# Performance work log

Hardware: AMD Instinct MI355X
Metric: run time of the kernel (lower is better)

The kernel has to match this reference:

```python
import jax, jax.numpy as jnp
import numpy as np

THETA = 0.02


def _low_texture_mask(tgt_img):
    # grad magnitudes averaged over channels
    gx = jnp.mean(jnp.abs(tgt_img[:, :, :, :-1] - tgt_img[:, :, :, 1:]), axis=1, keepdims=True)
    gy = jnp.mean(jnp.abs(tgt_img[:, :, :-1, :] - tgt_img[:, :, 1:, :]), axis=1, keepdims=True)
    tw = jnp.zeros_like(tgt_img[:, :1, :, :])
    tw = tw.at[:, :, :, :-1].add(gx)
    tw = tw.at[:, :, :-1, :].add(gy)
    tw = tw / 2.0
    return tw < jnp.mean(tw)  # [B,1,H,W] bool: low-texture == invalid


def _forward(pred_depth, gt_depth, tgt_img, u_rand):
    B, C, H, W = gt_depth.shape
    N = H * W
    invalid = _low_texture_mask(tgt_img).reshape(B, N)          # bool [B,N]
    valid = ~invalid
    gt = gt_depth.reshape(B, N)
    pred = pred_depth.reshape(B, N)

    # Uniform sampling among valid pixels per batch (inverse-CDF on cumsum).
    vcum = jnp.cumsum(valid.astype(jnp.int32), axis=1)          # [B,N]
    nval = vcum[:, -1:]                                         # [B,1]
    u = jnp.minimum((u_rand * nval.astype(u_rand.dtype)).astype(jnp.int32), nval - 1)
    idx = jax.vmap(lambda c, uu: jnp.searchsorted(c, uu, side='right'))(vcum, u)  # [B,N]

    gt_val = jnp.take_along_axis(gt, idx, axis=1)               # z_B ground truth
    pred_val = jnp.take_along_axis(pred, idx, axis=1)           # z_B prediction

    # Relative-depth target for (invalid pixel, sampled valid pixel) pairs
    r1 = gt / gt_val
    r2 = gt_val / gt
    target = jnp.where(r1 >= 1.0 + THETA, 1.0,
                       jnp.where(r2 > 1.0 + THETA, -1.0, 0.0))

    d = pred - pred_val                                         # z_A - z_B
    nz = invalid & (target != 0.0)
    zz = invalid & (target == 0.0)

    arg = jnp.where(nz, -target * d, 0.0)
    log_loss = jnp.sum(jnp.where(nz, jnp.log1p(jnp.exp(arg)), 0.0)) / jnp.sum(nz).astype(d.dtype)
    sq_loss = jnp.sum(jnp.where(zz, d * d, 0.0)) / jnp.sum(zz).astype(d.dtype)
    return log_loss + sq_loss


def setup_inputs() -> dict:
    key = jax.random.key(0)
    k1, k2, k3, k4 = jax.random.split(key, 4)
    B, H, W = 16, 512, 1024
    pred_depth = jax.random.normal(k1, (B, 1, H, W), dtype=jnp.float32)
    gt_depth = jax.random.uniform(k2, (B, 1, H, W), dtype=jnp.float32, minval=0.01, maxval=1.0)
    tgt_img = jax.random.uniform(k3, (B, 3, H, W), dtype=jnp.float32)
    u_rand = jax.random.uniform(k4, (B, H * W), dtype=jnp.float32)
    return {"pred_depth": pred_depth, "gt_depth": gt_depth, "tgt_img": tgt_img, "u_rand": u_rand}


def reference(pred_depth, gt_depth, tgt_img, u_rand):
    return _forward(pred_depth, gt_depth, tgt_img, u_rand)
```

## Files before the change

kernel.cpp:

```cpp
#include <hip/hip_runtime.h>
#include <hip/hip_bf16.h>
#include <math.h>

#define BB 16
#define CC 3
#define HH 512
#define WW 1024
#define NN (HH * WW)
#define BN ((size_t)BB * NN)

typedef __attribute__((ext_vector_type(4))) _Float16 half4;
typedef __attribute__((ext_vector_type(2))) _Float16 h2;
typedef __attribute__((ext_vector_type(4))) float f4;


__device__ __forceinline__ void tw4(const float* __restrict__ img, size_t g0, float out[4]) {
    int w0 = (int)(g0 & (WW - 1));
    int h  = (int)((g0 >> 10) & (HH - 1));
    int b  = (int)(g0 >> 19);
    const float* p = img + (size_t)b * CC * NN + (size_t)h * WW + w0;
    float c0[5], c1[5], c2[5], d0[4], d1[4], d2[4];
    f4 v;
    v = *(const f4*)p;            c0[0]=v.x; c0[1]=v.y; c0[2]=v.z; c0[3]=v.w;
    v = *(const f4*)(p + NN);     c1[0]=v.x; c1[1]=v.y; c1[2]=v.z; c1[3]=v.w;
    v = *(const f4*)(p + 2*NN);   c2[0]=v.x; c2[1]=v.y; c2[2]=v.z; c2[3]=v.w;
    bool haveR = (w0 < WW - 4);
    c0[4] = haveR ? p[4]        : 0.f;
    c1[4] = haveR ? p[NN + 4]   : 0.f;
    c2[4] = haveR ? p[2*NN + 4] : 0.f;
    bool haveD = (h < HH - 1);
    if (haveD) {
        v = *(const f4*)(p + WW);          d0[0]=v.x; d0[1]=v.y; d0[2]=v.z; d0[3]=v.w;
        v = *(const f4*)(p + NN + WW);     d1[0]=v.x; d1[1]=v.y; d1[2]=v.z; d1[3]=v.w;
        v = *(const f4*)(p + 2*NN + WW);   d2[0]=v.x; d2[1]=v.y; d2[2]=v.z; d2[3]=v.w;
    } else {
        #pragma unroll
        for (int j = 0; j < 4; ++j) { d0[j] = 0.f; d1[j] = 0.f; d2[j] = 0.f; }
    }
    #pragma unroll
    for (int j = 0; j < 4; ++j) {
        float tw = 0.f;
        if (w0 + j < WW - 1)
            tw += (fabsf(c0[j]-c0[j+1]) + fabsf(c1[j]-c1[j+1]) + fabsf(c2[j]-c2[j+1])) / 3.0f;
        if (haveD)
            tw += (fabsf(c0[j]-d0[j]) + fabsf(c1[j]-d1[j]) + fabsf(c2[j]-d2[j])) / 3.0f;
        out[j] = tw * 0.5f;
    }
}

__global__ __launch_bounds__(256) void tw_sum_kernel(const float* __restrict__ img,
                                                     double* __restrict__ sum_part,
                                                     _Float16* __restrict__ tw_out) {
    size_t g0 = ((size_t)blockIdx.x * 256 + threadIdx.x) * 4;
    float tw[4]; tw4(img, g0, tw);
    half4 hv; hv.x = (_Float16)tw[0]; hv.y = (_Float16)tw[1];
    hv.z = (_Float16)tw[2]; hv.w = (_Float16)tw[3];
    *(half4*)(tw_out + g0) = hv;
    double acc = (double)((tw[0] + tw[1]) + (tw[2] + tw[3]));
    int lane = threadIdx.x & 63, wid = threadIdx.x >> 6;
    for (int o = 32; o > 0; o >>= 1) acc += __shfl_down(acc, o);
    __shared__ double sd[4];
    if (lane == 0) sd[wid] = acc;
    __syncthreads();
    if (threadIdx.x == 0) atomicAdd(&sum_part[blockIdx.x & 63], sd[0]+sd[1]+sd[2]+sd[3]);
}

__global__ __launch_bounds__(256) void mask_kernel(const _Float16* __restrict__ tw_in,
                                                   const double* __restrict__ sum_part,
                                                   unsigned int* __restrict__ mask,
                                                   int* __restrict__ counts) {
    __shared__ float s_mean;
    __shared__ unsigned int wds[32];
    __shared__ int sv[4];
    int t = threadIdx.x;
    if (t == 0) {
        double s = 0.0;
        for (int i = 0; i < 64; ++i) s += sum_part[i];
        s_mean = (float)(s / (double)BN);
    }
    if (t < 32) wds[t] = 0;
    __syncthreads();
    float mean = s_mean;
    size_t g0 = ((size_t)blockIdx.x * 256 + t) * 4;
    half4 hv = *(const half4*)(tw_in + g0);
    unsigned int nib = ((float)hv.x < mean ? 1u : 0u) | ((float)hv.y < mean ? 2u : 0u)
                     | ((float)hv.z < mean ? 4u : 0u) | ((float)hv.w < mean ? 8u : 0u);
    atomicOr(&wds[t >> 3], nib << ((t & 7) * 4));
    int cv = 4 - __popc(nib);
    int lane = t & 63, wid = t >> 6;
    for (int o = 32; o > 0; o >>= 1) cv += __shfl_down(cv, o);
    if (lane == 0) sv[wid] = cv;
    __syncthreads();
    if (t < 32) mask[(size_t)blockIdx.x * 32 + t] = wds[t];
    if (t == 0) atomicAdd(&counts[blockIdx.x >> 3], sv[0]+sv[1]+sv[2]+sv[3]);
}

__global__ void scan_kernel(int* __restrict__ counts, int* __restrict__ nval) {
    int lane = threadIdx.x & 63;
    int row = threadIdx.x >> 6;
    int v = counts[row * 64 + lane];
    int incl = v;
    for (int o = 1; o < 64; o <<= 1) {
        int n = __shfl_up(incl, o);
        if (lane >= o) incl += n;
    }
    counts[row * 64 + lane] = incl - v;
    if (lane == 63) nval[row] = incl;
}

__global__ __launch_bounds__(256) void scatter_kernel(const unsigned int* __restrict__ mask,
                                                      const int* __restrict__ offsets,
                                                      const float* __restrict__ gt,
                                                      const float* __restrict__ pred,
                                                      h2* __restrict__ val) {
    int cglob = blockIdx.x;
    int b  = cglob >> 6;
    int t = threadIdx.x;
    __shared__ unsigned int svb[256];
    __shared__ int swoff[256];
    __shared__ int wsum[4];
    unsigned int vb = ~mask[(size_t)cglob * 256 + t];
    svb[t] = vb;
    int cnt = __popc(vb);
    int lane = t & 63, wid = t >> 6;
    int incl = cnt;
    for (int o = 1; o < 64; o <<= 1) {
        int n = __shfl_up(incl, o);
        if (lane >= o) incl += n;
    }
    if (lane == 63) wsum[wid] = incl;
    __syncthreads();
    int woff = 0;
    for (int i = 0; i < wid; i++) woff += wsum[i];
    swoff[t] = woff + incl - cnt;
    __syncthreads();
    size_t rowb = (size_t)b << 19;
    int chunkbase = offsets[cglob];
    size_t gbase = rowb + (size_t)(cglob & 63) * 8192;
    int bit = t & 31;
    unsigned int below = (bit == 0) ? 0u : ((1u << bit) - 1u);
    #pragma unroll 4
    for (int i = 0; i < 32; ++i) {
        int e = i * 256 + t;
        unsigned int bits = svb[i * 8 + (t >> 5)];
        if ((bits >> bit) & 1u) {
            int rank = chunkbase + swoff[i * 8 + (t >> 5)] + __popc(bits & below);
            size_t src = gbase + e;
            h2 o; o.x = (_Float16)gt[src]; o.y = (_Float16)pred[src];
            val[rowb + rank] = o;
        }
    }
}

__device__ __forceinline__ float fget(const f4& v, int k) {
    switch (k) { case 0: return v.x; case 1: return v.y; case 2: return v.z; default: return v.w; }
}

__global__ __launch_bounds__(256) void loss_kernel(const float* __restrict__ pred,
                                                   const float* __restrict__ gt,
                                                   const float* __restrict__ ur,
                                                   const unsigned int* __restrict__ mask,
                                                   const h2* __restrict__ val,
                                                   const int* __restrict__ nv_arr,
                                                   double* __restrict__ acc_ls,
                                                   double* __restrict__ acc_ss,
                                                   unsigned int* __restrict__ cnt_nz,
                                                   unsigned int* __restrict__ cnt_zz) {
    int t = threadIdx.x;
    int bid = blockIdx.x;
    int b = ((bid & 7) << 1) | ((bid >> 3) & 1);
    int chunk = bid >> 4;
    size_t rowb = (size_t)b << 19;
    int n0 = (chunk << 12) + t * 16;
    size_t g0 = rowb + (size_t)n0;
    unsigned int bits =
        (__builtin_nontemporal_load(&mask[g0 >> 5]) >> ((t & 1) << 4)) & 0xFFFFu;
    int nv = nv_arr[b];
    float fnv = (float)nv;
    f4 U[4], G[4], P[4];
    const f4* up = (const f4*)(ur + g0);
    const f4* gp = (const f4*)(gt + g0);
    const f4* pp = (const f4*)(pred + g0);
    #pragma unroll
    for (int i = 0; i < 4; ++i) {
        U[i] = __builtin_nontemporal_load(up + i);
        G[i] = __builtin_nontemporal_load(gp + i);
        P[i] = __builtin_nontemporal_load(pp + i);
    }
    float ls = 0.f, ss = 0.f;
    int cnz = 0, czz = 0;
    #pragma unroll
    for (int j = 0; j < 16; ++j) {
        if ((bits >> j) & 1u) {
            float urv = fget(U[j >> 2], j & 3);
            int u = min((int)(urv * fnv), nv - 1);
            h2 v = val[rowb + (size_t)u];
            float vx = (float)v.x, vy = (float)v.y;
            float gc = fget(G[j >> 2], j & 3);
            float pc = fget(P[j >> 2], j & 3);
            float d = pc - vy;
            if (gc >= 1.02f * vx)      { ls += __logf(1.f + __expf(-d)); ++cnz; }
            else if (vx > 1.02f * gc)  { ls += __logf(1.f + __expf( d)); ++cnz; }
            else                       { ss += d * d; ++czz; }
        }
    }
    int lane = t & 63, wid = t >> 6;
    __shared__ double sd[4];
    __shared__ unsigned int si[4];
    double lsd = (double)ls, ssd = (double)ss;
    for (int o = 32; o > 0; o >>= 1) lsd += __shfl_down(lsd, o);
    if (lane == 0) sd[wid] = lsd;
    __syncthreads();
    if (t == 0) atomicAdd(&acc_ls[bid & 63], sd[0]+sd[1]+sd[2]+sd[3]);
    __syncthreads();
    for (int o = 32; o > 0; o >>= 1) ssd += __shfl_down(ssd, o);
    if (lane == 0) sd[wid] = ssd;
    __syncthreads();
    if (t == 0) atomicAdd(&acc_ss[bid & 63], sd[0]+sd[1]+sd[2]+sd[3]);
    __syncthreads();
    for (int o = 32; o > 0; o >>= 1) cnz += __shfl_down(cnz, o);
    if (lane == 0) si[wid] = (unsigned int)cnz;
    __syncthreads();
    if (t == 0) atomicAdd(&cnt_nz[bid & 63], si[0]+si[1]+si[2]+si[3]);
    __syncthreads();
    for (int o = 32; o > 0; o >>= 1) czz += __shfl_down(czz, o);
    if (lane == 0) si[wid] = (unsigned int)czz;
    __syncthreads();
    if (t == 0) atomicAdd(&cnt_zz[bid & 63], si[0]+si[1]+si[2]+si[3]);
}

__global__ void finalize_kernel(const double* __restrict__ acc_ls,
                                const double* __restrict__ acc_ss,
                                const unsigned int* __restrict__ cnt_nz,
                                const unsigned int* __restrict__ cnt_zz,
                                float* __restrict__ out) {
    int t = threadIdx.x;
    double l = acc_ls[t], s2 = acc_ss[t];
    unsigned int a = cnt_nz[t], c = cnt_zz[t];
    for (int o = 32; o > 0; o >>= 1) {
        l  += __shfl_down(l, o);
        s2 += __shfl_down(s2, o);
        a  += __shfl_down(a, o);
        c  += __shfl_down(c, o);
    }
    if (t == 0) out[0] = (float)(l / (double)a + s2 / (double)c);
}

extern "C" void kernel_launch(void* const* d_in, const int* in_sizes, int n_in,
                              void* d_out, int out_size, void* d_ws, size_t ws_size,
                              hipStream_t stream) {
    const float* pred = (const float*)d_in[0];
    const float* gt   = (const float*)d_in[1];
    const float* img  = (const float*)d_in[2];
    const float* ur   = (const float*)d_in[3];
    float* out = (float*)d_out;

    char* ws = (char*)d_ws;
    double*       sum_part = (double*)(ws + 0);
    double*       acc_ls   = (double*)(ws + 512);
    double*       acc_ss   = (double*)(ws + 1024);
    unsigned int* cnt_nz   = (unsigned int*)(ws + 1536);
    unsigned int* cnt_zz   = (unsigned int*)(ws + 1792);
    int*          nval     = (int*)(ws + 2048);
    int*          counts   = (int*)(ws + 4096);
    unsigned int* mask     = (unsigned int*)(ws + 8192);
    h2*           val      = (h2*)(ws + (1 << 21));
    _Float16*     tw       = (_Float16*)(ws + (1 << 21));

    (void)hipMemsetAsync(ws, 0, 8192, stream);
    tw_sum_kernel <<<8192, 256, 0, stream>>>(img, sum_part, tw);
    mask_kernel   <<<8192, 256, 0, stream>>>(tw, sum_part, mask, counts);
    scan_kernel   <<<1, 1024, 0, stream>>>(counts, nval);
    scatter_kernel<<<1024, 256, 0, stream>>>(mask, counts, gt, pred, val);
    loss_kernel   <<<2048, 256, 0, stream>>>(pred, gt, ur, mask, val, nval,
                                             acc_ls, acc_ss, cnt_nz, cnt_zz);
    finalize_kernel<<<1, 64, 0, stream>>>(acc_ls, acc_ss, cnt_nz, cnt_zz, out);
}
```

Before: 126.1 us.

## Reuse row loads across rows in texture kernel; halve loss work per thread

The texture-gradient kernel now processes four consecutive rows per block, carrying the lower-neighbour row in registers as the next row's current row. This avoids reloading each image row twice and cuts redundant global traffic. Separately, the loss kernel now handles 8 pixels per thread with twice as many blocks, trading fewer loads in flight per thread for more parallelism on the gather-heavy loop.

```diff
diff --git a/kernel.cpp b/kernel.cpp
--- a/kernel.cpp
+++ b/kernel.cpp
@@ -8,61 +8,78 @@
 #define WW 1024
 #define NN (HH * WW)
 #define BN ((size_t)BB * NN)
+#define RPB 4
 
 typedef __attribute__((ext_vector_type(4))) _Float16 half4;
 typedef __attribute__((ext_vector_type(2))) _Float16 h2;
 typedef __attribute__((ext_vector_type(4))) float f4;
 
 
-__device__ __forceinline__ void tw4(const float* __restrict__ img, size_t g0, float out[4]) {
-    int w0 = (int)(g0 & (WW - 1));
-    int h  = (int)((g0 >> 10) & (HH - 1));
-    int b  = (int)(g0 >> 19);
-    const float* p = img + (size_t)b * CC * NN + (size_t)h * WW + w0;
-    float c0[5], c1[5], c2[5], d0[4], d1[4], d2[4];
-    f4 v;
-    v = *(const f4*)p;            c0[0]=v.x; c0[1]=v.y; c0[2]=v.z; c0[3]=v.w;
-    v = *(const f4*)(p + NN);     c1[0]=v.x; c1[1]=v.y; c1[2]=v.z; c1[3]=v.w;
-    v = *(const f4*)(p + 2*NN);   c2[0]=v.x; c2[1]=v.y; c2[2]=v.z; c2[3]=v.w;
-    bool haveR = (w0 < WW - 4);
-    c0[4] = haveR ? p[4]        : 0.f;
-    c1[4] = haveR ? p[NN + 4]   : 0.f;
-    c2[4] = haveR ? p[2*NN + 4] : 0.f;
-    bool haveD = (h < HH - 1);
-    if (haveD) {
-        v = *(const f4*)(p + WW);          d0[0]=v.x; d0[1]=v.y; d0[2]=v.z; d0[3]=v.w;
-        v = *(const f4*)(p + NN + WW);     d1[0]=v.x; d1[1]=v.y; d1[2]=v.z; d1[3]=v.w;
-        v = *(const f4*)(p + 2*NN + WW);   d2[0]=v.x; d2[1]=v.y; d2[2]=v.z; d2[3]=v.w;
-    } else {
-        #pragma unroll
-        for (int j = 0; j < 4; ++j) { d0[j] = 0.f; d1[j] = 0.f; d2[j] = 0.f; }
-    }
-    #pragma unroll
-    for (int j = 0; j < 4; ++j) {
-        float tw = 0.f;
-        if (w0 + j < WW - 1)
-            tw += (fabsf(c0[j]-c0[j+1]) + fabsf(c1[j]-c1[j+1]) + fabsf(c2[j]-c2[j+1])) / 3.0f;
-        if (haveD)
-            tw += (fabsf(c0[j]-d0[j]) + fabsf(c1[j]-d1[j]) + fabsf(c2[j]-d2[j])) / 3.0f;
-        out[j] = tw * 0.5f;
-    }
-}
-
 __global__ __launch_bounds__(256) void tw_sum_kernel(const float* __restrict__ img,
                                                      double* __restrict__ sum_part,
                                                      _Float16* __restrict__ tw_out) {
-    size_t g0 = ((size_t)blockIdx.x * 256 + threadIdx.x) * 4;
-    float tw[4]; tw4(img, g0, tw);
-    half4 hv; hv.x = (_Float16)tw[0]; hv.y = (_Float16)tw[1];
-    hv.z = (_Float16)tw[2]; hv.w = (_Float16)tw[3];
-    *(half4*)(tw_out + g0) = hv;
-    double acc = (double)((tw[0] + tw[1]) + (tw[2] + tw[3]));
-    int lane = threadIdx.x & 63, wid = threadIdx.x >> 6;
+    int t = threadIdx.x;
+    int bid = blockIdx.x;
+    int b = bid >> 7;
+    int h0 = (bid & 127) * RPB;
+    const float* base = img + (size_t)b * CC * NN;
+    int w0 = t * 4;
+    bool haveR = (w0 < WW - 4);
+    size_t rb = (size_t)h0 * WW + w0;
+    f4 c0 = *(const f4*)(base + rb);
+    f4 c1 = *(const f4*)(base + NN + rb);
+    f4 c2 = *(const f4*)(base + 2 * NN + rb);
+    float e0 = haveR ? base[rb + 4] : 0.f;
+    float e1 = haveR ? base[NN + rb + 4] : 0.f;
+    float e2 = haveR ? base[2 * NN + rb + 4] : 0.f;
+    float rowacc = 0.f;
+    #pragma unroll
+    for (int r = 0; r < RPB; ++r) {
+        int h = h0 + r;
+        bool haveD = (h < HH - 1);
+        size_t db = (size_t)(h + 1) * WW + w0;
+        f4 d0, d1, d2;
+        float f0, f1, f2;
+        if (haveD) {
+            d0 = *(const f4*)(base + db);
+            d1 = *(const f4*)(base + NN + db);
+            d2 = *(const f4*)(base + 2 * NN + db);
+            f0 = haveR ? base[db + 4] : 0.f;
+            f1 = haveR ? base[NN + db + 4] : 0.f;
+            f2 = haveR ? base[2 * NN + db + 4] : 0.f;
+        } else {
+            d0 = d1 = d2 = (f4)0.f;
+            f0 = f1 = f2 = 0.f;
+        }
+        float a0[5] = {c0.x, c0.y, c0.z, c0.w, e0};
+        float a1[5] = {c1.x, c1.y, c1.z, c1.w, e1};
+        float a2[5] = {c2.x, c2.y, c2.z, c2.w, e2};
+        float b0[4] = {d0.x, d0.y, d0.z, d0.w};
+        float b1[4] = {d1.x, d1.y, d1.z, d1.w};
+        float b2[4] = {d2.x, d2.y, d2.z, d2.w};
+        float tw[4];
+        #pragma unroll
+        for (int j = 0; j < 4; ++j) {
+            float twv = 0.f;
+            if (w0 + j < WW - 1)
+                twv += (fabsf(a0[j]-a0[j+1]) + fabsf(a1[j]-a1[j+1]) + fabsf(a2[j]-a2[j+1])) / 3.0f;
+            if (haveD)
+                twv += (fabsf(a0[j]-b0[j]) + fabsf(a1[j]-b1[j]) + fabsf(a2[j]-b2[j])) / 3.0f;
+            tw[j] = twv * 0.5f;
+        }
+        half4 hv; hv.x = (_Float16)tw[0]; hv.y = (_Float16)tw[1];
+        hv.z = (_Float16)tw[2]; hv.w = (_Float16)tw[3];
+        *(half4*)(tw_out + (size_t)b * NN + (size_t)h * WW + w0) = hv;
+        rowacc += (tw[0] + tw[1]) + (tw[2] + tw[3]);
+        c0 = d0; c1 = d1; c2 = d2; e0 = f0; e1 = f1; e2 = f2;
+    }
+    double acc = (double)rowacc;
+    int lane = t & 63, wid = t >> 6;
     for (int o = 32; o > 0; o >>= 1) acc += __shfl_down(acc, o);
     __shared__ double sd[4];
     if (lane == 0) sd[wid] = acc;
     __syncthreads();
-    if (threadIdx.x == 0) atomicAdd(&sum_part[blockIdx.x & 63], sd[0]+sd[1]+sd[2]+sd[3]);
+    if (t == 0) atomicAdd(&sum_part[bid & 63], sd[0]+sd[1]+sd[2]+sd[3]);
 }
 
 __global__ __launch_bounds__(256) void mask_kernel(const _Float16* __restrict__ tw_in,
@@ -171,18 +188,18 @@
     int b = ((bid & 7) << 1) | ((bid >> 3) & 1);
     int chunk = bid >> 4;
     size_t rowb = (size_t)b << 19;
-    int n0 = (chunk << 12) + t * 16;
+    int n0 = (chunk << 11) + t * 8;
     size_t g0 = rowb + (size_t)n0;
     unsigned int bits =
-        (__builtin_nontemporal_load(&mask[g0 >> 5]) >> ((t & 1) << 4)) & 0xFFFFu;
+        (__builtin_nontemporal_load(&mask[g0 >> 5]) >> ((t & 3) << 3)) & 0xFFu;
     int nv = nv_arr[b];
     float fnv = (float)nv;
-    f4 U[4], G[4], P[4];
+    f4 U[2], G[2], P[2];
     const f4* up = (const f4*)(ur + g0);
     const f4* gp = (const f4*)(gt + g0);
     const f4* pp = (const f4*)(pred + g0);
     #pragma unroll
-    for (int i = 0; i < 4; ++i) {
+    for (int i = 0; i < 2; ++i) {
         U[i] = __builtin_nontemporal_load(up + i);
         G[i] = __builtin_nontemporal_load(gp + i);
         P[i] = __builtin_nontemporal_load(pp + i);
@@ -190,7 +207,7 @@
     float ls = 0.f, ss = 0.f;
     int cnz = 0, czz = 0;
     #pragma unroll
-    for (int j = 0; j < 16; ++j) {
+    for (int j = 0; j < 8; ++j) {
         if ((bits >> j) & 1u) {
             float urv = fget(U[j >> 2], j & 3);
             int u = min((int)(urv * fnv), nv - 1);
@@ -268,11 +285,11 @@
     _Float16*     tw       = (_Float16*)(ws + (1 << 21));
 
     (void)hipMemsetAsync(ws, 0, 8192, stream);
-    tw_sum_kernel <<<8192, 256, 0, stream>>>(img, sum_part, tw);
+    tw_sum_kernel <<<2048, 256, 0, stream>>>(img, sum_part, tw);
     mask_kernel   <<<8192, 256, 0, stream>>>(tw, sum_part, mask, counts);
     scan_kernel   <<<1, 1024, 0, stream>>>(counts, nval);
     scatter_kernel<<<1024, 256, 0, stream>>>(mask, counts, gt, pred, val);
-    loss_kernel   <<<2048, 256, 0, stream>>>(pred, gt, ur, mask, val, nval,
+    loss_kernel   <<<4096, 256, 0, stream>>>(pred, gt, ur, mask, val, nval,
                                              acc_ls, acc_ss, cnt_nz, cnt_zz);
     finalize_kernel<<<1, 64, 0, stream>>>(acc_ls, acc_ss, cnt_nz, cnt_zz, out);
 }
```

After: 111.1 us. -11.9%, faster.
